# Kernel tuning notes

Hardware: AMD Instinct MI355X
Metric: run time of the kernel (lower is better)

The kernel has to match this reference:

```python
import jax, jax.numpy as jnp
from jax import lax
import numpy as np

B, T, E, H, ENC, V = 64, 49, 512, 512, 1024, 32000


def setup_inputs() -> dict:
    key = jax.random.key(0)
    ks = jax.random.split(key, 12)
    embeddings = jax.random.normal(ks[0], (B, T, E), jnp.float32)
    encoder_out = jax.random.normal(ks[1], (B, ENC), jnp.float32)
    # caption lengths sorted descending (module assumes this for ragged truncation)
    lens = jax.random.randint(ks[2], (B,), 10, T + 2)
    caption_lengths = jnp.sort(lens)[::-1]
    caption_lengths = caption_lengths.at[0].set(T + 1)  # max decode length == T
    s = 1.0 / np.sqrt(H)
    u = lambda k, shp, lim: jax.random.uniform(k, shp, jnp.float32, -lim, lim)
    W_ih = u(ks[3], (4 * H, E), s)
    W_hh = u(ks[4], (4 * H, H), s)
    b_ih = u(ks[5], (4 * H,), s)
    b_hh = u(ks[6], (4 * H,), s)
    se = 1.0 / np.sqrt(ENC)
    W_init_h = u(ks[7], (H, ENC), se)
    b_init_h = u(ks[8], (H,), se)
    W_init_c = u(ks[9], (H, ENC), se)
    b_init_c = u(ks[10], (H,), se)
    W_fc = u(ks[11], (V, H), 0.1)  # init_weights: uniform(-0.1, 0.1)
    b_fc = jnp.zeros((V,), jnp.float32)
    return dict(embeddings=embeddings, encoder_out=encoder_out,
                caption_lengths=caption_lengths,
                W_ih=W_ih, W_hh=W_hh, b_ih=b_ih, b_hh=b_hh,
                W_init_h=W_init_h, b_init_h=b_init_h,
                W_init_c=W_init_c, b_init_c=b_init_c,
                W_fc=W_fc, b_fc=b_fc)


def reference(embeddings, encoder_out, caption_lengths,
              W_ih, W_hh, b_ih, b_hh,
              W_init_h, b_init_h, W_init_c, b_init_c,
              W_fc, b_fc):
    # dropout is treated as identity (eval mode) for the deterministic reference
    h0 = encoder_out @ W_init_h.T + b_init_h  # [B, H]
    c0 = encoder_out @ W_init_c.T + b_init_c
    decode_lengths = caption_lengths - 1
    Tn = embeddings.shape[1]
    # mask[t, b] = True iff example b is still active at step t
    mask = jnp.arange(Tn)[:, None] < decode_lengths[None, :]  # [T, B]
    xs = jnp.transpose(embeddings, (1, 0, 2))  # [T, B, E]

    def step(carry, inp):
        h, c = carry
        x, m = inp
        gates = x @ W_ih.T + b_ih + h @ W_hh.T + b_hh  # [B, 4H]
        i, f, g, o = jnp.split(gates, 4, axis=-1)
        i = jax.nn.sigmoid(i); f = jax.nn.sigmoid(f)
        g = jnp.tanh(g); o = jax.nn.sigmoid(o)
        c_new = f * c + i * g
        h_new = o * jnp.tanh(c_new)
        preds = h_new @ W_fc.T + b_fc  # [B, V]
        m2 = m[:, None]
        # inactive rows: state frozen (torch only updates h[:batch_size_t]),
        # predictions stay zero
        h = jnp.where(m2, h_new, h)
        c = jnp.where(m2, c_new, c)
        preds = jnp.where(m2, preds, 0.0)
        return (h, c), preds

    (_, _), preds = lax.scan(step, (h0, c0), (xs, mask))
    predictions = jnp.transpose(preds, (1, 0, 2))  # [B, T, V]
    return predictions, decode_lengths
```

## Files before the change

kernel.cpp:

```cpp
#include <hip/hip_runtime.h>
#include <stdint.h>

#define B_    64
#define T_    49
#define E_    512
#define H_    512
#define ENC_  1024
#define V_    32000
#define G4_   2048
#define M_    3136
#define MPAD_ 3200
#define NPROD 32
#define NWG   256
#define NTN   250

typedef __attribute__((ext_vector_type(8))) short bf16x8;
typedef __attribute__((ext_vector_type(4))) float f32x4;

static __device__ __forceinline__ unsigned short f2bf(float f) {
  union { float f; uint32_t u; } v; v.f = f;
  uint32_t r = v.u + 0x7FFFu + ((v.u >> 16) & 1u);
  return (unsigned short)(r >> 16);
}

static __device__ __forceinline__ void async16(const void* g, void* lds) {
  __builtin_amdgcn_global_load_lds(
      (const __attribute__((address_space(1))) unsigned int*)g,
      (__attribute__((address_space(3))) unsigned int*)lds, 16, 0, 0);
}

static __device__ __forceinline__ float sigf(float x) { return 1.0f / (1.0f + expf(-x)); }

__global__ __launch_bounds__(256) void convert_kernel(
    const float* __restrict__ Wih, const float* __restrict__ Whh,
    const float* __restrict__ emb,
    unsigned short* __restrict__ WihB, unsigned short* __restrict__ WhhB,
    unsigned short* __restrict__ AxB) {
  const int n_wih = (G4_ * E_) / 4;
  const int n_whh = (G4_ * H_) / 4;
  const int n_emb = (B_ * T_ * E_) / 4;
  const int n_pad = ((MPAD_ - M_) * E_) / 4;
  const long total = (long)n_wih + n_whh + n_emb + n_pad;
  for (long u = (long)blockIdx.x * blockDim.x + threadIdx.x; u < total;
       u += (long)gridDim.x * blockDim.x) {
    long i = u;
    if (i < n_wih) {
      float4 v = ((const float4*)Wih)[i];
      ushort4 o; o.x = f2bf(v.x); o.y = f2bf(v.y); o.z = f2bf(v.z); o.w = f2bf(v.w);
      ((ushort4*)WihB)[i] = o; continue;
    }
    i -= n_wih;
    if (i < n_whh) {
      float4 v = ((const float4*)Whh)[i];
      ushort4 o; o.x = f2bf(v.x); o.y = f2bf(v.y); o.z = f2bf(v.z); o.w = f2bf(v.w);
      ((ushort4*)WhhB)[i] = o; continue;
    }
    i -= n_whh;
    if (i < n_emb) {
      int bt = (int)(i >> 7);
      int e4 = (int)(i & 127);
      int b = bt / T_, t = bt - b * T_;
      float4 v = ((const float4*)emb)[i];
      ushort4 o; o.x = f2bf(v.x); o.y = f2bf(v.y); o.z = f2bf(v.z); o.w = f2bf(v.w);
      ((ushort4*)AxB)[((long)(t * 64 + b) << 7) + e4] = o; continue;
    }
    i -= n_emb;
    ushort4 z; z.x = z.y = z.z = z.w = 0;
    ((ushort4*)AxB)[((long)M_ << 7) + i] = z;
  }
}

__global__ __launch_bounds__(256) void init_kernel(
    const float* __restrict__ enc, const int* __restrict__ cap,
    const float* __restrict__ Wh, const float* __restrict__ bh,
    const float* __restrict__ Wc, const float* __restrict__ bc,
    unsigned short* __restrict__ h0b, float* __restrict__ c0,
    float* __restrict__ out_dl, int* __restrict__ meta,
    int* __restrict__ rowmap, int* __restrict__ zrowmap) {
  __shared__ __align__(16) float e[ENC_];
  __shared__ int s_nb[T_];
  __shared__ int s_start[T_ + 1];
  const int b = blockIdx.x, q = blockIdx.y, tid = threadIdx.x;
  ((float4*)e)[tid] = ((const float4*)(enc + (size_t)b * ENC_))[tid];
  __syncthreads();
  const bool is_c = tid >= 128;
  const int j = q * 128 + (tid & 127);
  const float* W = is_c ? Wc : Wh;
  float s = is_c ? bc[j] : bh[j];
  const float4* wr = (const float4*)(W + (size_t)j * ENC_);
  const float4* e4 = (const float4*)e;
#pragma unroll 4
  for (int k = 0; k < ENC_ / 4; ++k) {
    float4 w = wr[k], v = e4[k];
    s += w.x * v.x + w.y * v.y + w.z * v.z + w.w * v.w;
  }
  if (is_c) c0[(size_t)b * H_ + j] = s;
  else      h0b[(size_t)b * H_ + j] = f2bf(s);
  if (b == 0 && q == 0 && tid < B_) out_dl[tid] = (float)(cap[tid] - 1);

  if (b == 0 && q == 0) {
    __syncthreads();
    if (tid < T_) {
      int cnt = 0;
      for (int bb = 0; bb < B_; ++bb) cnt += (cap[bb] - 1 > tid) ? 1 : 0;
      s_nb[tid] = cnt;
    }
    __syncthreads();
    if (tid == 0) {
      int acc = 0;
      for (int t = 0; t < T_; ++t) { s_start[t] = acc; acc += s_nb[t]; }
      s_start[T_] = acc;
      const int Mc = acc;
      const int MT = (Mc + 127) >> 7;
      meta[100] = Mc;
      meta[101] = MT;
      meta[104] = M_ - Mc;
      meta[105] = NTN + (M_ - Mc) + MT * NTN;
      for (int i = Mc; i < MT * 128; ++i) rowmap[i] = -1;
    }
    __syncthreads();
    if (tid < T_) {
      meta[tid] = s_start[tid];
      const int st = s_start[tid], nb = s_nb[tid];
      for (int bb = 0; bb < nb; ++bb) rowmap[st + bb] = bb * T_ + tid;
      int zst = 0;
      for (int t2 = 0; t2 < tid; ++t2) zst += B_ - s_nb[t2];
      for (int bb = nb; bb < B_; ++bb) zrowmap[zst + (bb - nb)] = bb * T_ + tid;
    }
    __syncthreads();
    if (tid < 26) {
      const int Mc = s_start[T_];
      const int MT = (Mc + 127) >> 7;
      if (tid < MT) {
        int last = tid * 128 + 127;
        if (last > Mc - 1) last = Mc - 1;
        int tlast = 0;
        for (int t2 = 0; t2 < T_; ++t2) if (s_start[t2] <= last) tlast = t2;
        meta[110 + tid] = tlast + 1;
      }
    }
  }
}

__global__ __launch_bounds__(256) void pad_kernel(const int* __restrict__ meta,
                                                  unsigned short* __restrict__ Hall) {
  const int Mc = meta[100], MT = meta[101];
  const int tot = (MT * 128 - Mc) * 64;
  for (int i = blockIdx.x * blockDim.x + threadIdx.x; i < tot;
       i += gridDim.x * blockDim.x) {
    const int row = Mc + (i >> 6), c = i & 63;
    ushort4 z; z.x = z.y = z.z = z.w = 0;
    *(ushort4*)((char*)Hall + (size_t)row * 1024 + c * 16) = z;
  }
}

__global__ __launch_bounds__(256) void gemm_gx(
    const unsigned short* __restrict__ A, const unsigned short* __restrict__ Bm,
    float* __restrict__ C, const float* __restrict__ bias0, const float* __restrict__ bias1) {
  __shared__ __align__(16) char smem[65536];
  const int tid = threadIdx.x, lane = tid & 63, wid = tid >> 6;
  const int nt = blockIdx.x, mt = blockIdx.y;
  const int wr = wid >> 1, wc = wid & 1;
  const int m0 = mt * 128, n0 = nt * 128;
  f32x4 acc[4][4] = {};

  auto stage = [&](int buf, int kit) {
    const int k0b = kit * 128;
#pragma unroll
    for (int i = 0; i < 4; ++i) {
      int chunk = wid * 4 + i;
      int d = chunk * 1024 + lane * 16;
      int row = d >> 7, colb = d & 127;
      int sc = colb ^ ((row & 7) << 4);
      async16((const char*)A + (size_t)(m0 + row) * 1024 + k0b + sc,
              smem + buf * 16384 + chunk * 1024);
      async16((const char*)Bm + (size_t)(n0 + row) * 1024 + k0b + sc,
              smem + 32768 + buf * 16384 + chunk * 1024);
    }
  };

  stage(0, 0);
  __syncthreads();
  for (int kit = 0; kit < 8; ++kit) {
    const int buf = kit & 1;
    if (kit < 7) stage(buf ^ 1, kit + 1);
    const char* Ab = smem + buf * 16384;
    const char* Bb = smem + 32768 + buf * 16384;
#pragma unroll
    for (int kb = 0; kb < 2; ++kb) {
      const int colb = kb * 64 + (lane >> 4) * 16;
      bf16x8 af[4], bfb[4];
#pragma unroll
      for (int rt = 0; rt < 4; ++rt) {
        int ar = wr * 64 + rt * 16 + (lane & 15);
        af[rt] = *(const bf16x8*)(Ab + ar * 128 + (colb ^ ((ar & 7) << 4)));
        int br = wc * 64 + rt * 16 + (lane & 15);
        bfb[rt] = *(const bf16x8*)(Bb + br * 128 + (colb ^ ((br & 7) << 4)));
      }
#pragma unroll
      for (int i = 0; i < 4; ++i)
#pragma unroll
        for (int j = 0; j < 4; ++j)
          acc[i][j] = __builtin_amdgcn_mfma_f32_16x16x32_bf16(af[i], bfb[j], acc[i][j], 0, 0, 0);
    }
    __syncthreads();
  }
#pragma unroll
  for (int i = 0; i < 4; ++i) {
    const int rbase = m0 + wr * 64 + i * 16 + (lane >> 4) * 4;
#pragma unroll
    for (int j = 0; j < 4; ++j) {
      const int col = n0 + wc * 64 + j * 16 + (lane & 15);
#pragma unroll
      for (int r = 0; r < 4; ++r)
        C[(size_t)(rbase + r) * G4_ + col] = acc[i][j][r] + bias0[col] + bias1[col];
    }
  }
}

__global__ __launch_bounds__(512, 1) void fused_kernel(
    const float* __restrict__ Gx, const unsigned short* __restrict__ WhhB,
    const unsigned short* __restrict__ h0b, const float* __restrict__ c0,
    unsigned short* __restrict__ hsl, unsigned short* __restrict__ Hall,
    const float* __restrict__ Wfc, unsigned short* __restrict__ WfcB,
    const float* __restrict__ bfc, const int* __restrict__ cap,
    float* __restrict__ outp, int* __restrict__ ctrl, const int* __restrict__ meta,
    const int* __restrict__ rowmap, const int* __restrict__ zrowmap) {
  __shared__ __align__(16) char smem[131072];
  const int tid = threadIdx.x, lane = tid & 63, wid = tid >> 6;
  int* s_tile = (int*)(smem + 131068);
  int* s_role = (int*)(smem + 131064);

  {
    int xcc;
    asm volatile("s_getreg_b32 %0, hwreg(HW_REG_XCC_ID)" : "=s"(xcc));
    if (tid == 0) {
      xcc &= 7;
      int a = __hip_atomic_fetch_add(&ctrl[592 + xcc * 16], 1, __ATOMIC_RELAXED,
                                     __HIP_MEMORY_SCOPE_AGENT);
      if (a == NPROD - 1) {
        int expected = 0;
        __hip_atomic_compare_exchange_strong(&ctrl[560], &expected, xcc + 1,
                                             __ATOMIC_RELAXED, __ATOMIC_RELAXED,
                                             __HIP_MEMORY_SCOPE_AGENT);
      }
      int e;
      for (;;) {
        e = __hip_atomic_load(&ctrl[560], __ATOMIC_RELAXED, __HIP_MEMORY_SCOPE_AGENT);
        if (e) break;
        __builtin_amdgcn_s_sleep(2);
      }
      int slot = NPROD;
      if (e - 1 == xcc)
        slot = __hip_atomic_fetch_add(&ctrl[576], 1, __ATOMIC_RELAXED,
                                      __HIP_MEMORY_SCOPE_AGENT);
      *s_role = slot;
    }
    __syncthreads();
  }
  const int w = *s_role;
  __syncthreads();

  if (w < NPROD) {
    __builtin_amdgcn_s_setprio(1);
    const int hc0 = w * 16;
    const bool act = tid < 256;
    const int g = wid;
    const int chunk_hi = lane >> 5;
    bf16x8 wf[16];
    f32x4 creg = {};
    ushort4 hold = {};
    int b = 0, hq = 0, hc = 0, dl = 0, myoff = 0;
    int arb[4] = {};
    if (act) {
      const int gcol = g * 512 + hc0 + (lane & 15);
      const int ko = (lane >> 4) * 8;
#pragma unroll
      for (int kb = 0; kb < 16; ++kb)
        wf[kb] = *(const bf16x8*)&WhhB[(size_t)gcol * 512 + kb * 32 + ko];
      b = tid >> 2; hq = (tid & 3) * 4; hc = hc0 + hq;
      dl = cap[b] - 1;
      creg = *(const f32x4*)&c0[b * H_ + hc];
      hold = *(const ushort4*)&h0b[b * H_ + hc];
      myoff = ((b * 32) ^ (((b >> 2) & 7) << 4) ^ ((hq >> 3) << 4)) + ((hq & 7) * 2);
      union { ushort4 s; unsigned long long u; } cv; cv.s = hold;
      *(unsigned long long*)((char*)hsl + w * 2048 + myoff) = cv.u;
#pragma unroll
      for (int rt = 0; rt < 4; ++rt) {
        int ar = rt * 16 + (lane & 15);
        arb[rt] = (ar * 32) ^ (((ar >> 2) & 7) << 4) ^ (((lane >> 4) & 1) << 4);
      }
    }
    float (*gl)[64][16] = (float (*)[64][16])(smem + 65536);
    asm volatile("s_waitcnt vmcnt(0)" ::: "memory");
    __syncthreads();
    if (tid == 0)
      __hip_atomic_store(&ctrl[w * 16], 1, __ATOMIC_RELAXED, __HIP_MEMORY_SCOPE_AGENT);

    for (int t = 0; t < T_; ++t) {
      f32x4 xi = {}, xf = {}, xg = {}, xo = {};
      if (act) {
        const size_t gxr = ((size_t)t * 64 + b) * (size_t)G4_ + hc;
        xi = *(const f32x4*)&Gx[gxr + 0];
        xf = *(const f32x4*)&Gx[gxr + 512];
        xg = *(const f32x4*)&Gx[gxr + 1024];
        xo = *(const f32x4*)&Gx[gxr + 1536];
      }
      __builtin_amdgcn_sched_barrier(0);
      if (tid < 64) {
        const int need = t + 1;
        for (;;) {
          int v = (lane < NPROD)
                      ? __hip_atomic_load(&ctrl[lane * 16], __ATOMIC_RELAXED, __HIP_MEMORY_SCOPE_AGENT)
                      : need;
          if (__all(v >= need)) break;
          __builtin_amdgcn_s_sleep(1);
        }
        if (tid == 0 && w == 0 && t > 0)
          __hip_atomic_store(&ctrl[512], t, __ATOMIC_RELAXED, __HIP_MEMORY_SCOPE_AGENT);
      }
      __syncthreads();
      {
        const char* src = (const char*)hsl + (t & 1) * 65536 + tid * 16;
        char* dst = smem + tid * 16;
        int4 hv[8];
#pragma unroll
        for (int i = 0; i < 8; ++i)
          asm volatile("global_load_dwordx4 %0, %1, off sc0"
                       : "=&v"(hv[i]) : "v"(src + i * 8192));
        asm volatile("s_waitcnt vmcnt(0)" ::: "memory");
#pragma unroll
        for (int i = 0; i < 8; ++i)
          *(int4*)(dst + i * 8192) = hv[i];
      }
      __syncthreads();
      if (act) {
        f32x4 accp[4] = {};
#pragma unroll
        for (int kb = 0; kb < 16; ++kb) {
          const int cbase = (kb * 2 + chunk_hi) * 2048;
#pragma unroll
          for (int rt = 0; rt < 4; ++rt) {
            bf16x8 af = *(const bf16x8*)(smem + cbase + arb[rt]);
            accp[rt] = __builtin_amdgcn_mfma_f32_16x16x32_bf16(af, wf[kb], accp[rt], 0, 0, 0);
          }
        }
#pragma unroll
        for (int rt = 0; rt < 4; ++rt)
#pragma unroll
          for (int r = 0; r < 4; ++r)
            gl[g][rt * 16 + (lane >> 4) * 4 + r][lane & 15] = accp[rt][r];
      }
      __syncthreads();
      if (act) {
        f32x4 vi = xi + *(const f32x4*)&gl[0][b][hq];
        f32x4 vf = xf + *(const f32x4*)&gl[1][b][hq];
        f32x4 vg = xg + *(const f32x4*)&gl[2][b][hq];
        f32x4 vo = xo + *(const f32x4*)&gl[3][b][hq];
        f32x4 cn;
        ushort4 hb16;
        {
          float hv4[4];
#pragma unroll
          for (int k = 0; k < 4; ++k) {
            float iv = sigf(vi[k]), fv = sigf(vf[k]), gv = tanhf(vg[k]), ov = sigf(vo[k]);
            cn[k] = fv * creg[k] + iv * gv;
            hv4[k] = ov * tanhf(cn[k]);
          }
          hb16.x = f2bf(hv4[0]); hb16.y = f2bf(hv4[1]); hb16.z = f2bf(hv4[2]); hb16.w = f2bf(hv4[3]);
        }
        if (t < dl) {
          union { ushort4 s; unsigned long long u; } cv; cv.s = hb16;
          __hip_atomic_store((unsigned long long*)&Hall[((size_t)(meta[t] + b)) * H_ + hc],
                             cv.u, __ATOMIC_RELAXED, __HIP_MEMORY_SCOPE_AGENT);
          hold = hb16; creg = cn;
        }
        if (t + 1 < T_) {
          union { ushort4 s; unsigned long long u; } cv; cv.s = hold;
          *(unsigned long long*)((char*)hsl + ((t + 1) & 1) * 65536 + w * 2048 + myoff) = cv.u;
        }
      }
      asm volatile("s_waitcnt vmcnt(0)" ::: "memory");
      __syncthreads();
      if (tid == 0)
        __hip_atomic_store(&ctrl[w * 16], t + 2, __ATOMIC_RELAXED, __HIP_MEMORY_SCOPE_AGENT);
    }
    if (w == 0 && tid < 64) {
      const int need = T_ + 1;
      for (;;) {
        int v = (lane < NPROD)
                    ? __hip_atomic_load(&ctrl[lane * 16], __ATOMIC_RELAXED, __HIP_MEMORY_SCOPE_AGENT)
                    : need;
        if (__all(v >= need)) break;
        __builtin_amdgcn_s_sleep(1);
      }
      if (tid == 0)
        __hip_atomic_store(&ctrl[512], T_, __ATOMIC_RELAXED, __HIP_MEMORY_SCOPE_AGENT);
    }
    __builtin_amdgcn_s_setprio(0);
  }

  const int NZI = meta[104];
  const int NTOT = meta[105];
  const int wr = wid >> 2, wc = wid & 3;
  for (;;) {
    __syncthreads();
    if (tid == 0)
      *s_tile = __hip_atomic_fetch_add(&ctrl[528], 1, __ATOMIC_RELAXED, __HIP_MEMORY_SCOPE_AGENT);
    __syncthreads();
    const int tile = *s_tile;
    __syncthreads();
    if (tile >= NTOT) break;

    if (tile < NTN) {
      const float4* src = (const float4*)(Wfc + (size_t)tile * 128 * 512);
      unsigned long long* dst = (unsigned long long*)WfcB + (size_t)tile * 16384;
      for (int i = tid; i < 16384; i += 512) {
        float4 v = src[i];
        union { ushort4 s; unsigned long long u; } cv;
        cv.s.x = f2bf(v.x); cv.s.y = f2bf(v.y); cv.s.z = f2bf(v.z); cv.s.w = f2bf(v.w);
        __hip_atomic_store(&dst[i], cv.u, __ATOMIC_RELAXED, __HIP_MEMORY_SCOPE_AGENT);
      }
      asm volatile("s_waitcnt vmcnt(0)" ::: "memory");
      __syncthreads();
      if (tid == 0)
        __hip_atomic_fetch_add(&ctrl[544], 1, __ATOMIC_RELAXED, __HIP_MEMORY_SCOPE_AGENT);
      continue;
    }

    if (tile < NTN + NZI) {
      const int bt = zrowmap[tile - NTN];
      f32x4* dst = (f32x4*)(outp + (size_t)bt * V_);
      f32x4 z = {0.0f, 0.0f, 0.0f, 0.0f};
      for (int i = tid; i < V_ / 4; i += 512) dst[i] = z;
      continue;
    }

    const int gt = tile - NTN - NZI;
    const int mt = gt / NTN, nt = gt - mt * NTN;
    const int m0 = mt * 128, n0 = nt * 128;
    const int need = meta[110 + mt];
    if (tid == 0) {
      while (__hip_atomic_load(&ctrl[544], __ATOMIC_RELAXED, __HIP_MEMORY_SCOPE_AGENT) < NTN)
        __builtin_amdgcn_s_sleep(2);
      while (__hip_atomic_load(&ctrl[512], __ATOMIC_RELAXED, __HIP_MEMORY_SCOPE_AGENT) < need)
        __builtin_amdgcn_s_sleep(8);
    }
    __syncthreads();

    f32x4 acc[4][2] = {};
    auto stage = [&](int buf, int kit) {
      const int k0b = kit * 128;
#pragma unroll
      for (int i = 0; i < 2; ++i) {
        int chunk = wid * 2 + i;
        int d = chunk * 1024 + lane * 16;
        int row = d >> 7, colb = d & 127;
        int sc = colb ^ ((row & 7) << 4);
        async16((const char*)Hall + (size_t)(m0 + row) * 1024 + k0b + sc,
                smem + buf * 16384 + chunk * 1024);
        async16((const char*)WfcB + (size_t)(n0 + row) * 1024 + k0b + sc,
                smem + 32768 + buf * 16384 + chunk * 1024);
      }
    };
    stage(0, 0);
    __syncthreads();
    for (int kit = 0; kit < 8; ++kit) {
      const int buf = kit & 1;
      if (kit < 7) stage(buf ^ 1, kit + 1);
      const char* Ab = smem + buf * 16384;
      const char* Bb = smem + 32768 + buf * 16384;
#pragma unroll
      for (int kb = 0; kb < 2; ++kb) {
        const int colb = kb * 64 + (lane >> 4) * 16;
        bf16x8 bfb[2];
#pragma unroll
        for (int j = 0; j < 2; ++j) {
          int br = wc * 32 + j * 16 + (lane & 15);
          bfb[j] = *(const bf16x8*)(Bb + br * 128 + (colb ^ ((br & 7) << 4)));
        }
#pragma unroll
        for (int rt = 0; rt < 4; ++rt) {
          int ar = wr * 64 + rt * 16 + (lane & 15);
          bf16x8 af = *(const bf16x8*)(Ab + ar * 128 + (colb ^ ((ar & 7) << 4)));
#pragma unroll
          for (int j = 0; j < 2; ++j)
            acc[rt][j] = __builtin_amdgcn_mfma_f32_16x16x32_bf16(af, bfb[j], acc[rt][j], 0, 0, 0);
        }
      }
      __syncthreads();
    }
    float* Ct = (float*)smem;
#pragma unroll
    for (int j = 0; j < 2; ++j) {
      const int colL = wc * 32 + j * 16 + (lane & 15);
      const float bz = bfc[n0 + colL];
#pragma unroll
      for (int rt = 0; rt < 4; ++rt) {
        const int rb = wr * 64 + rt * 16 + (lane >> 4) * 4;
#pragma unroll
        for (int r = 0; r < 4; ++r) {
          const int row = rb + r;
          Ct[row * 128 + (colL ^ ((row & 7) << 2))] = acc[rt][j][r] + bz;
        }
      }
    }
    __syncthreads();
    const int c4 = tid & 31;
    const int rsub = tid >> 5;
#pragma unroll
    for (int itr = 0; itr < 8; ++itr) {
      const int row = itr * 16 + rsub;
      const int bt = rowmap[m0 + row];
      if (bt < 0) continue;
      f32x4 v = *(const f32x4*)&Ct[row * 128 + ((c4 ^ (row & 7)) << 2)];
      *(f32x4*)(outp + (size_t)bt * V_ + n0 + (c4 << 2)) = v;
    }
  }
}

extern "C" void kernel_launch(void* const* d_in, const int* in_sizes, int n_in,
                              void* d_out, int out_size, void* d_ws, size_t ws_size,
                              hipStream_t stream) {
  const float* emb = (const float*)d_in[0];
  const float* enc = (const float*)d_in[1];
  const int*   cap = (const int*)d_in[2];
  const float* Wih = (const float*)d_in[3];
  const float* Whh = (const float*)d_in[4];
  const float* bih = (const float*)d_in[5];
  const float* bhh = (const float*)d_in[6];
  const float* Wh0 = (const float*)d_in[7];
  const float* bh0 = (const float*)d_in[8];
  const float* Wc0 = (const float*)d_in[9];
  const float* bc0 = (const float*)d_in[10];
  const float* Wfc = (const float*)d_in[11];
  const float* bfc = (const float*)d_in[12];
  float* out = (float*)d_out;

  char* ws = (char*)d_ws;
  size_t o = 0;
  auto carve = [&](size_t bytes) { void* p = ws + o; o += (bytes + 255) & ~(size_t)255; return p; };
  unsigned short* WihB = (unsigned short*)carve((size_t)G4_ * E_ * 2);
  unsigned short* WhhB = (unsigned short*)carve((size_t)G4_ * H_ * 2);
  unsigned short* WfcB = (unsigned short*)carve((size_t)V_ * H_ * 2);
  unsigned short* AxB  = (unsigned short*)carve((size_t)MPAD_ * E_ * 2);
  float*          Gx   = (float*)carve((size_t)MPAD_ * G4_ * 4);
  unsigned short* Hall = (unsigned short*)carve((size_t)MPAD_ * H_ * 2);
  unsigned short* h0b  = (unsigned short*)carve((size_t)B_ * H_ * 2);
  float*          cst  = (float*)carve((size_t)B_ * H_ * 4);
  unsigned short* hsl  = (unsigned short*)carve((size_t)2 * 65536);
  int*            ctrl = (int*)carve(4096);
  int*            meta = (int*)carve(1024);
  int*            rowmap = (int*)carve((size_t)MPAD_ * 4);
  int*            zrowmap = (int*)carve((size_t)MPAD_ * 4);
  (void)ws_size; (void)in_sizes; (void)n_in; (void)out_size;

  hipMemsetAsync(ctrl, 0, 4096, stream);
  convert_kernel<<<dim3(1024), dim3(256), 0, stream>>>(Wih, Whh, emb, WihB, WhhB, AxB);
  init_kernel<<<dim3(64, 4), dim3(256), 0, stream>>>(enc, cap, Wh0, bh0, Wc0, bc0, h0b, cst,
                                                     out + (size_t)B_ * T_ * V_,
                                                     meta, rowmap, zrowmap);
  pad_kernel<<<dim3(32), dim3(256), 0, stream>>>(meta, Hall);
  gemm_gx<<<dim3(G4_ / 128, MPAD_ / 128), dim3(256), 0, stream>>>(AxB, WihB, Gx, bih, bhh);
  fused_kernel<<<dim3(NWG), dim3(512), 0, stream>>>(Gx, WhhB, h0b, cst, hsl, Hall,
                                                    Wfc, WfcB, bfc, cap, out, ctrl,
                                                    meta, rowmap, zrowmap);
}
```

Before: 387.4 us.

## Halve recurrent producer workgroups, add scatter workgroups, store Gx in bf16

Cuts the LSTM recurrence producers from 32 to 16 workgroups, each now using all 8 waves over 32 hidden columns, so each per-step grid barrier polls fewer flags. A separate group of 8 scatter workgroups copies h from a triple-buffered staging area into Hall, taking global writes and ragged row mapping off the critical path, and the FC tiles now wait on their progress flags. The input-gate precompute Gx is stored as bf16 to halve its memory traffic. This lowers Gx precision and adds a third sync role that can add scheduling latency.

```diff
diff --git a/kernel.cpp b/kernel.cpp
--- a/kernel.cpp
+++ b/kernel.cpp
@@ -10,7 +10,8 @@
 #define G4_   2048
 #define M_    3136
 #define MPAD_ 3200
-#define NPROD 32
+#define NPROD 16
+#define NSCR  8
 #define NWG   256
 #define NTN   250
 
@@ -21,6 +22,9 @@
   union { float f; uint32_t u; } v; v.f = f;
   uint32_t r = v.u + 0x7FFFu + ((v.u >> 16) & 1u);
   return (unsigned short)(r >> 16);
+}
+static __device__ __forceinline__ float bf2f(unsigned short u) {
+  union { uint32_t i; float f; } c; c.i = (uint32_t)u << 16; return c.f;
 }
 
 static __device__ __forceinline__ void async16(const void* g, void* lds) {
@@ -156,7 +160,8 @@
 
 __global__ __launch_bounds__(256) void gemm_gx(
     const unsigned short* __restrict__ A, const unsigned short* __restrict__ Bm,
-    float* __restrict__ C, const float* __restrict__ bias0, const float* __restrict__ bias1) {
+    unsigned short* __restrict__ C, const float* __restrict__ bias0,
+    const float* __restrict__ bias1) {
   __shared__ __align__(16) char smem[65536];
   const int tid = threadIdx.x, lane = tid & 63, wid = tid >> 6;
   const int nt = blockIdx.x, mt = blockIdx.y;
@@ -211,15 +216,16 @@
 #pragma unroll
     for (int j = 0; j < 4; ++j) {
       const int col = n0 + wc * 64 + j * 16 + (lane & 15);
+      const float bz = bias0[col] + bias1[col];
 #pragma unroll
       for (int r = 0; r < 4; ++r)
-        C[(size_t)(rbase + r) * G4_ + col] = acc[i][j][r] + bias0[col] + bias1[col];
+        C[(size_t)(rbase + r) * G4_ + col] = f2bf(acc[i][j][r] + bz);
     }
   }
 }
 
 __global__ __launch_bounds__(512, 1) void fused_kernel(
-    const float* __restrict__ Gx, const unsigned short* __restrict__ WhhB,
+    const unsigned short* __restrict__ GxB, const unsigned short* __restrict__ WhhB,
     const unsigned short* __restrict__ h0b, const float* __restrict__ c0,
     unsigned short* __restrict__ hsl, unsigned short* __restrict__ Hall,
     const float* __restrict__ Wfc, unsigned short* __restrict__ WfcB,
@@ -238,7 +244,7 @@
       xcc &= 7;
       int a = __hip_atomic_fetch_add(&ctrl[592 + xcc * 16], 1, __ATOMIC_RELAXED,
                                      __HIP_MEMORY_SCOPE_AGENT);
-      if (a == NPROD - 1) {
+      if (a == NPROD + NSCR - 1) {
         int expected = 0;
         __hip_atomic_compare_exchange_strong(&ctrl[560], &expected, xcc + 1,
                                              __ATOMIC_RELAXED, __ATOMIC_RELAXED,
@@ -250,7 +256,7 @@
         if (e) break;
         __builtin_amdgcn_s_sleep(2);
       }
-      int slot = NPROD;
+      int slot = 1000;
       if (e - 1 == xcc)
         slot = __hip_atomic_fetch_add(&ctrl[576], 1, __ATOMIC_RELAXED,
                                       __HIP_MEMORY_SCOPE_AGENT);
@@ -263,34 +269,31 @@
 
   if (w < NPROD) {
     __builtin_amdgcn_s_setprio(1);
-    const int hc0 = w * 16;
-    const bool act = tid < 256;
-    const int g = wid;
+    const int hc0 = w * 32;
+    const int gcol = (wid >> 1) * 512 + hc0 + (wid & 1) * 16 + (lane & 15);
+    const int ko = (lane >> 4) * 8;
+    bf16x8 wf[16];
+#pragma unroll
+    for (int kb = 0; kb < 16; ++kb)
+      wf[kb] = *(const bf16x8*)&WhhB[(size_t)gcol * 512 + kb * 32 + ko];
+    const int b = tid >> 3, hq = (tid & 7) * 4, hc = hc0 + hq;
+    const int dl = cap[b] - 1;
+    f32x4 creg = *(const f32x4*)&c0[b * H_ + hc];
+    ushort4 hold = *(const ushort4*)&h0b[b * H_ + hc];
+    const int myoff = w * 4096 + (hq >> 4) * 2048 +
+                      ((b * 32) ^ (((b >> 2) & 7) << 4) ^ (((hq >> 3) & 1) << 4)) +
+                      (hq & 7) * 2;
+    {
+      union { ushort4 s; unsigned long long u; } cv; cv.s = hold;
+      *(unsigned long long*)((char*)hsl + myoff) = cv.u;
+    }
+    int arb[4];
+#pragma unroll
+    for (int rt = 0; rt < 4; ++rt) {
+      int ar = rt * 16 + (lane & 15);
+      arb[rt] = (ar * 32) ^ (((ar >> 2) & 7) << 4) ^ (((lane >> 4) & 1) << 4);
+    }
     const int chunk_hi = lane >> 5;
-    bf16x8 wf[16];
-    f32x4 creg = {};
-    ushort4 hold = {};
-    int b = 0, hq = 0, hc = 0, dl = 0, myoff = 0;
-    int arb[4] = {};
-    if (act) {
-      const int gcol = g * 512 + hc0 + (lane & 15);
-      const int ko = (lane >> 4) * 8;
-#pragma unroll
-      for (int kb = 0; kb < 16; ++kb)
-        wf[kb] = *(const bf16x8*)&WhhB[(size_t)gcol * 512 + kb * 32 + ko];
-      b = tid >> 2; hq = (tid & 3) * 4; hc = hc0 + hq;
-      dl = cap[b] - 1;
-      creg = *(const f32x4*)&c0[b * H_ + hc];
-      hold = *(const ushort4*)&h0b[b * H_ + hc];
-      myoff = ((b * 32) ^ (((b >> 2) & 7) << 4) ^ ((hq >> 3) << 4)) + ((hq & 7) * 2);
-      union { ushort4 s; unsigned long long u; } cv; cv.s = hold;
-      *(unsigned long long*)((char*)hsl + w * 2048 + myoff) = cv.u;
-#pragma unroll
-      for (int rt = 0; rt < 4; ++rt) {
-        int ar = rt * 16 + (lane & 15);
-        arb[rt] = (ar * 32) ^ (((ar >> 2) & 7) << 4) ^ (((lane >> 4) & 1) << 4);
-      }
-    }
     float (*gl)[64][16] = (float (*)[64][16])(smem + 65536);
     asm volatile("s_waitcnt vmcnt(0)" ::: "memory");
     __syncthreads();
@@ -298,30 +301,26 @@
       __hip_atomic_store(&ctrl[w * 16], 1, __ATOMIC_RELAXED, __HIP_MEMORY_SCOPE_AGENT);
 
     for (int t = 0; t < T_; ++t) {
-      f32x4 xi = {}, xf = {}, xg = {}, xo = {};
-      if (act) {
-        const size_t gxr = ((size_t)t * 64 + b) * (size_t)G4_ + hc;
-        xi = *(const f32x4*)&Gx[gxr + 0];
-        xf = *(const f32x4*)&Gx[gxr + 512];
-        xg = *(const f32x4*)&Gx[gxr + 1024];
-        xo = *(const f32x4*)&Gx[gxr + 1536];
-      }
+      const size_t gxr = ((size_t)t * 64 + b) * (size_t)G4_ + hc0 + hq;
+      ushort4 gx0 = *(const ushort4*)&GxB[gxr + 0];
+      ushort4 gx1 = *(const ushort4*)&GxB[gxr + 512];
+      ushort4 gx2 = *(const ushort4*)&GxB[gxr + 1024];
+      ushort4 gx3 = *(const ushort4*)&GxB[gxr + 1536];
       __builtin_amdgcn_sched_barrier(0);
       if (tid < 64) {
-        const int need = t + 1;
+        const int need_p = t + 1;
+        const int need_s = (t >= 2) ? (t - 2) : 0;
         for (;;) {
-          int v = (lane < NPROD)
-                      ? __hip_atomic_load(&ctrl[lane * 16], __ATOMIC_RELAXED, __HIP_MEMORY_SCOPE_AGENT)
-                      : need;
+          int v = 0x7fffffff, need = 0;
+          if (lane < NPROD) { v = __hip_atomic_load(&ctrl[lane * 16], __ATOMIC_RELAXED, __HIP_MEMORY_SCOPE_AGENT); need = need_p; }
+          else if (lane < NPROD + NSCR) { v = __hip_atomic_load(&ctrl[lane * 16], __ATOMIC_RELAXED, __HIP_MEMORY_SCOPE_AGENT); need = need_s; }
           if (__all(v >= need)) break;
           __builtin_amdgcn_s_sleep(1);
         }
-        if (tid == 0 && w == 0 && t > 0)
-          __hip_atomic_store(&ctrl[512], t, __ATOMIC_RELAXED, __HIP_MEMORY_SCOPE_AGENT);
       }
       __syncthreads();
       {
-        const char* src = (const char*)hsl + (t & 1) * 65536 + tid * 16;
+        const char* src = (const char*)hsl + (t % 3) * 65536 + tid * 16;
         char* dst = smem + tid * 16;
         int4 hv[8];
 #pragma unroll
@@ -334,7 +333,7 @@
           *(int4*)(dst + i * 8192) = hv[i];
       }
       __syncthreads();
-      if (act) {
+      {
         f32x4 accp[4] = {};
 #pragma unroll
         for (int kb = 0; kb < 16; ++kb) {
@@ -349,55 +348,74 @@
         for (int rt = 0; rt < 4; ++rt)
 #pragma unroll
           for (int r = 0; r < 4; ++r)
-            gl[g][rt * 16 + (lane >> 4) * 4 + r][lane & 15] = accp[rt][r];
-      }
-      __syncthreads();
-      if (act) {
-        f32x4 vi = xi + *(const f32x4*)&gl[0][b][hq];
-        f32x4 vf = xf + *(const f32x4*)&gl[1][b][hq];
-        f32x4 vg = xg + *(const f32x4*)&gl[2][b][hq];
-        f32x4 vo = xo + *(const f32x4*)&gl[3][b][hq];
+            gl[wid][rt * 16 + (lane >> 4) * 4 + r][lane & 15] = accp[rt][r];
+      }
+      __syncthreads();
+      {
+        const int wsel = hq >> 4, ci = hq & 15;
+        f32x4 vi = *(const f32x4*)&gl[0 + wsel][b][ci];
+        f32x4 vf = *(const f32x4*)&gl[2 + wsel][b][ci];
+        f32x4 vg = *(const f32x4*)&gl[4 + wsel][b][ci];
+        f32x4 vo = *(const f32x4*)&gl[6 + wsel][b][ci];
+        vi[0] += bf2f(gx0.x); vi[1] += bf2f(gx0.y); vi[2] += bf2f(gx0.z); vi[3] += bf2f(gx0.w);
+        vf[0] += bf2f(gx1.x); vf[1] += bf2f(gx1.y); vf[2] += bf2f(gx1.z); vf[3] += bf2f(gx1.w);
+        vg[0] += bf2f(gx2.x); vg[1] += bf2f(gx2.y); vg[2] += bf2f(gx2.z); vg[3] += bf2f(gx2.w);
+        vo[0] += bf2f(gx3.x); vo[1] += bf2f(gx3.y); vo[2] += bf2f(gx3.z); vo[3] += bf2f(gx3.w);
         f32x4 cn;
         ushort4 hb16;
-        {
-          float hv4[4];
-#pragma unroll
-          for (int k = 0; k < 4; ++k) {
-            float iv = sigf(vi[k]), fv = sigf(vf[k]), gv = tanhf(vg[k]), ov = sigf(vo[k]);
-            cn[k] = fv * creg[k] + iv * gv;
-            hv4[k] = ov * tanhf(cn[k]);
-          }
-          hb16.x = f2bf(hv4[0]); hb16.y = f2bf(hv4[1]); hb16.z = f2bf(hv4[2]); hb16.w = f2bf(hv4[3]);
-        }
-        if (t < dl) {
-          union { ushort4 s; unsigned long long u; } cv; cv.s = hb16;
-          __hip_atomic_store((unsigned long long*)&Hall[((size_t)(meta[t] + b)) * H_ + hc],
-                             cv.u, __ATOMIC_RELAXED, __HIP_MEMORY_SCOPE_AGENT);
-          hold = hb16; creg = cn;
-        }
-        if (t + 1 < T_) {
-          union { ushort4 s; unsigned long long u; } cv; cv.s = hold;
-          *(unsigned long long*)((char*)hsl + ((t + 1) & 1) * 65536 + w * 2048 + myoff) = cv.u;
-        }
+        float hv4[4];
+#pragma unroll
+        for (int k = 0; k < 4; ++k) {
+          float iv = sigf(vi[k]), fv = sigf(vf[k]), gv = tanhf(vg[k]), ov = sigf(vo[k]);
+          cn[k] = fv * creg[k] + iv * gv;
+          hv4[k] = ov * tanhf(cn[k]);
+        }
+        hb16.x = f2bf(hv4[0]); hb16.y = f2bf(hv4[1]); hb16.z = f2bf(hv4[2]); hb16.w = f2bf(hv4[3]);
+        if (t < dl) { hold = hb16; creg = cn; }
+        union { ushort4 s; unsigned long long u; } cv; cv.s = hold;
+        *(unsigned long long*)((char*)hsl + ((t + 1) % 3) * 65536 + myoff) = cv.u;
       }
       asm volatile("s_waitcnt vmcnt(0)" ::: "memory");
       __syncthreads();
       if (tid == 0)
         __hip_atomic_store(&ctrl[w * 16], t + 2, __ATOMIC_RELAXED, __HIP_MEMORY_SCOPE_AGENT);
     }
-    if (w == 0 && tid < 64) {
-      const int need = T_ + 1;
-      for (;;) {
-        int v = (lane < NPROD)
-                    ? __hip_atomic_load(&ctrl[lane * 16], __ATOMIC_RELAXED, __HIP_MEMORY_SCOPE_AGENT)
-                    : need;
-        if (__all(v >= need)) break;
-        __builtin_amdgcn_s_sleep(1);
-      }
+    __builtin_amdgcn_s_setprio(0);
+  } else if (w < NPROD + NSCR) {
+    const int s = w - NPROD;
+    const int r8 = tid >> 6;
+    const int b = s * 8 + r8;
+    const int l = lane;
+    const int srcoff = (l >> 2) * 4096 + ((l >> 1) & 1) * 2048 +
+                       ((b * 32) ^ (((b >> 2) & 7) << 4) ^ ((l & 1) << 4));
+    for (int tau = 1; tau <= T_; ++tau) {
+      if (tid < 64) {
+        for (;;) {
+          int v = (lane < NPROD)
+                      ? __hip_atomic_load(&ctrl[lane * 16], __ATOMIC_RELAXED, __HIP_MEMORY_SCOPE_AGENT)
+                      : (tau + 1);
+          if (__all(v >= tau + 1)) break;
+          __builtin_amdgcn_s_sleep(1);
+        }
+      }
+      __syncthreads();
+      const int st = meta[tau - 1];
+      const int nb = ((tau < T_) ? meta[tau] : meta[100]) - st;
+      if (b < nb) {
+        int4 hv;
+        const char* src = (const char*)hsl + (tau % 3) * 65536 + srcoff;
+        asm volatile("global_load_dwordx4 %0, %1, off sc0" : "=&v"(hv) : "v"(src));
+        asm volatile("s_waitcnt vmcnt(0)" ::: "memory");
+        union { int4 v; unsigned long long u[2]; } cv; cv.v = hv;
+        unsigned long long* dst = (unsigned long long*)&Hall[(size_t)(st + b) * H_ + l * 8];
+        __hip_atomic_store(&dst[0], cv.u[0], __ATOMIC_RELAXED, __HIP_MEMORY_SCOPE_AGENT);
+        __hip_atomic_store(&dst[1], cv.u[1], __ATOMIC_RELAXED, __HIP_MEMORY_SCOPE_AGENT);
+      }
+      asm volatile("s_waitcnt vmcnt(0)" ::: "memory");
+      __syncthreads();
       if (tid == 0)
-        __hip_atomic_store(&ctrl[512], T_, __ATOMIC_RELAXED, __HIP_MEMORY_SCOPE_AGENT);
-    }
-    __builtin_amdgcn_s_setprio(0);
+        __hip_atomic_store(&ctrl[w * 16], tau, __ATOMIC_RELAXED, __HIP_MEMORY_SCOPE_AGENT);
+    }
   }
 
   const int NZI = meta[104];
@@ -443,8 +461,15 @@
     if (tid == 0) {
       while (__hip_atomic_load(&ctrl[544], __ATOMIC_RELAXED, __HIP_MEMORY_SCOPE_AGENT) < NTN)
         __builtin_amdgcn_s_sleep(2);
-      while (__hip_atomic_load(&ctrl[512], __ATOMIC_RELAXED, __HIP_MEMORY_SCOPE_AGENT) < need)
+    }
+    if (tid < 64) {
+      for (;;) {
+        int v = (lane < NSCR)
+                    ? __hip_atomic_load(&ctrl[(NPROD + lane) * 16], __ATOMIC_RELAXED, __HIP_MEMORY_SCOPE_AGENT)
+                    : need;
+        if (__all(v >= need)) break;
         __builtin_amdgcn_s_sleep(8);
+      }
     }
     __syncthreads();
 
@@ -544,11 +569,11 @@
   unsigned short* WhhB = (unsigned short*)carve((size_t)G4_ * H_ * 2);
   unsigned short* WfcB = (unsigned short*)carve((size_t)V_ * H_ * 2);
   unsigned short* AxB  = (unsigned short*)carve((size_t)MPAD_ * E_ * 2);
-  float*          Gx   = (float*)carve((size_t)MPAD_ * G4_ * 4);
+  unsigned short* GxB  = (unsigned short*)carve((size_t)MPAD_ * G4_ * 2);
   unsigned short* Hall = (unsigned short*)carve((size_t)MPAD_ * H_ * 2);
   unsigned short* h0b  = (unsigned short*)carve((size_t)B_ * H_ * 2);
   float*          cst  = (float*)carve((size_t)B_ * H_ * 4);
-  unsigned short* hsl  = (unsigned short*)carve((size_t)2 * 65536);
+  unsigned short* hsl  = (unsigned short*)carve((size_t)3 * 65536);
   int*            ctrl = (int*)carve(4096);
   int*            meta = (int*)carve(1024);
   int*            rowmap = (int*)carve((size_t)MPAD_ * 4);
@@ -561,8 +586,8 @@
                                                      out + (size_t)B_ * T_ * V_,
                                                      meta, rowmap, zrowmap);
   pad_kernel<<<dim3(32), dim3(256), 0, stream>>>(meta, Hall);
-  gemm_gx<<<dim3(G4_ / 128, MPAD_ / 128), dim3(256), 0, stream>>>(AxB, WihB, Gx, bih, bhh);
-  fused_kernel<<<dim3(NWG), dim3(512), 0, stream>>>(Gx, WhhB, h0b, cst, hsl, Hall,
+  gemm_gx<<<dim3(G4_ / 128, MPAD_ / 128), dim3(256), 0, stream>>>(AxB, WihB, GxB, bih, bhh);
+  fused_kernel<<<dim3(NWG), dim3(512), 0, stream>>>(GxB, WhhB, h0b, cst, hsl, Hall,
                                                     Wfc, WfcB, bfc, cap, out, ctrl,
                                                     meta, rowmap, zrowmap);
 }
```

Result: no change. 380.4 us (-1.8%).
